# Optimization experiments

Hardware: AMD Instinct MI355X
Metric: run time of the kernel (lower is better)

## Reference

```python
import jax, jax.numpy as jnp
import numpy as np

N_NODES, N_EDGES = 10000, 160000
MUL0, MUL1 = 64, 32  # multiplicities of 0e and 1o in irreps_in
AVG_DEGREE = 16.0

# ---- real-basis Wigner 3j symbols (unit Frobenius norm, as in e3nn) ----
def _su2_gen(l):
    m = np.arange(-l, l + 1)
    Jz = np.diag(m).astype(complex)
    c = np.sqrt(l * (l + 1) - m[:-1] * (m[:-1] + 1))
    Jp = np.zeros((2 * l + 1, 2 * l + 1), complex)
    Jp[np.arange(1, 2 * l + 1), np.arange(2 * l)] = c
    Jm = Jp.conj().T
    return (Jp + Jm) / 2, (Jp - Jm) / 2j, Jz

def _c2r(l):
    U = np.zeros((2 * l + 1, 2 * l + 1), complex)
    s2 = 1 / np.sqrt(2)
    for m in range(-l, l + 1):
        if m > 0:
            U[l + m, l - m] = s2; U[l + m, l + m] = (-1) ** m * s2
        elif m == 0:
            U[l, l] = 1.0
        else:
            U[l + m, l + m] = 1j * s2; U[l + m, l - m] = -1j * (-1) ** m * s2
    return U

def _real_gen(l):
    U = _c2r(l)
    return [np.real(U @ (-1j * J) @ U.conj().T) for J in _su2_gen(l)]

def real_w3j(l1, l2, l3):
    A1, A2, A3 = _real_gen(l1), _real_gen(l2), _real_gen(l3)
    d1, d2, d3 = 2 * l1 + 1, 2 * l2 + 1, 2 * l3 + 1
    I1, I2, I3 = np.eye(d1), np.eye(d2), np.eye(d3)
    M = np.concatenate([
        np.kron(np.kron(A1[k], I2), I3) + np.kron(np.kron(I1, A2[k]), I3)
        + np.kron(np.kron(I1, I2), A3[k]) for k in range(3)], 0)
    v = np.linalg.svd(M)[2][-1]
    v = v / np.linalg.norm(v)
    nz = np.nonzero(np.abs(v) > 1e-8)[0][0]
    if v[nz] < 0:
        v = -v
    return jnp.asarray(v.reshape(d1, d2, d3), dtype=jnp.float32)

W000 = real_w3j(0, 0, 0); W011 = real_w3j(0, 1, 1); W022 = real_w3j(0, 2, 2)
W101 = real_w3j(1, 0, 1); W110 = real_w3j(1, 1, 0); W112 = real_w3j(1, 1, 2)
W121 = real_w3j(1, 2, 1)

# silu second-moment normalization constant (e3nn normalize2mom)
_x, _w = np.polynomial.hermite_e.hermegauss(128)
_s = _x / (1 + np.exp(-_x))
SILU_C = float(1.0 / np.sqrt((_w * _s ** 2).sum() / _w.sum()))
SQ3, SQ5 = float(np.sqrt(3.0)), float(np.sqrt(5.0))


def _forward(node_input, node_attr, edge_attr, edge_length_embedded,
             sc_w0, sc_w1, lin1_w0, lin1_w1, fc_w0, fc_w1,
             lin2_w0, lin2_w1, lin2_w2, edge_src, edge_dst):
    N = node_input.shape[0]
    E = edge_attr.shape[0]
    a = node_attr  # [N,1] scalar (0e) node attribute
    x0 = node_input[:, :MUL0]                       # [N,64]  0e block
    x1 = node_input[:, MUL0:].reshape(N, MUL1, 3)   # [N,32,3] 1o block

    # self connection sc = FullyConnectedTensorProduct(in, attr, out); no 2e path
    s0 = (x0 @ sc_w0) * a / jnp.sqrt(float(MUL0))
    s1 = jnp.einsum('nui,uv->nvi', x1, sc_w1) * a[:, :, None] / jnp.sqrt(float(MUL1))
    s = jnp.concatenate([s0, s1.reshape(N, -1),
                         jnp.zeros((N, 32 * 5), node_input.dtype)], 1)  # [N,320]

    # lin1 = FullyConnectedTensorProduct(in, attr, in)
    y0 = (x0 @ lin1_w0) * a / jnp.sqrt(float(MUL0))
    y1 = jnp.einsum('nui,uv->nvi', x1, lin1_w1) * a[:, :, None] / jnp.sqrt(float(MUL1))

    # radial FC net -> per-edge tensor-product weights [E,320]
    h = jax.nn.silu(edge_length_embedded @ fc_w0 / jnp.sqrt(8.0)) * SILU_C
    w = h @ fc_w1 / jnp.sqrt(64.0)

    xs0 = y0[edge_src][:, :, None]  # [E,64,1]
    xs1 = y1[edge_src]              # [E,32,3]
    e0, e1, e2 = edge_attr[:, :1], edge_attr[:, 1:4], edge_attr[:, 4:9]

    def path(x, e, wgt, C, pw):
        # x:[E,u,d1] e:[E,d2] wgt:[E,u] C:[d1,d2,d3] -> [E,u,d3]
        return pw * jnp.einsum('eui,ej,ijk,eu->euk', x, e, C, wgt)

    # 7 'uvu' instructions; weight slices in instruction order, outputs in sorted
    # irreps_mid order: 64x0e,32x0e,64x1o,32x1o,32x1o,64x2e,32x2e
    k0 = path(xs0, e0, w[:, 0:64],    W000, 1.0)   # 0e x 0e -> 0e, mul 64
    k2 = path(xs0, e1, w[:, 64:128],  W011, SQ3)   # 0e x 1o -> 1o, mul 64
    k5 = path(xs0, e2, w[:, 128:192], W022, SQ5)   # 0e x 2e -> 2e, mul 64
    k3 = path(xs1, e0, w[:, 192:224], W101, SQ3)   # 1o x 0e -> 1o, mul 32
    k1 = path(xs1, e1, w[:, 224:256], W110, 1.0)   # 1o x 1o -> 0e, mul 32
    k6 = path(xs1, e1, w[:, 256:288], W112, SQ5)   # 1o x 1o -> 2e, mul 32
    k4 = path(xs1, e2, w[:, 288:320], W121, SQ3)   # 1o x 2e -> 1o, mul 32
    edge_feat = jnp.concatenate(
        [k0.reshape(E, -1), k1.reshape(E, -1), k2.reshape(E, -1), k3.reshape(E, -1),
         k4.reshape(E, -1), k5.reshape(E, -1), k6.reshape(E, -1)], 1)  # [E,960]

    agg = jax.ops.segment_sum(edge_feat, edge_dst, num_segments=N) / jnp.sqrt(AVG_DEGREE)

    # lin2 = FullyConnectedTensorProduct(mid, attr, out); per-l fused matmuls
    m0 = agg[:, :96]                        # 0e muls 64+32
    m1 = agg[:, 96:480].reshape(N, 128, 3)  # 1o muls 64+32+32
    m2 = agg[:, 480:960].reshape(N, 96, 5)  # 2e muls 64+32
    o0 = (m0 @ lin2_w0) * a / jnp.sqrt(96.0)
    o1 = jnp.einsum('nui,uv->nvi', m1, lin2_w1) * a[:, :, None] / jnp.sqrt(128.0)
    o2 = jnp.einsum('nui,uv->nvi', m2, lin2_w2) * a[:, :, None] / jnp.sqrt(96.0)
    xo = jnp.concatenate([o0, o1.reshape(N, -1), o2.reshape(N, -1)], 1)  # [N,320]

    c_s = jnp.sin(jnp.pi / 8)
    c_x = jnp.cos(jnp.pi / 8)
    mask = jnp.concatenate([jnp.ones(160), jnp.zeros(160)]).astype(node_input.dtype)
    return c_s * s + (1.0 - mask + c_x * mask) * xo


def setup_inputs() -> dict:
    key = jax.random.key(0)
    ks = jax.random.split(key, 16)
    f = jax.random.normal
    return {
        'node_input': f(ks[0], (N_NODES, 160), jnp.float32),
        'node_attr': jnp.ones((N_NODES, 1), jnp.float32),
        'edge_src': jax.random.randint(ks[1], (N_EDGES,), 0, N_NODES, dtype=jnp.int32),
        'edge_dst': jax.random.randint(ks[2], (N_EDGES,), 0, N_NODES, dtype=jnp.int32),
        'edge_attr': f(ks[3], (N_EDGES, 9), jnp.float32),
        'edge_length_embedded': jax.random.uniform(ks[4], (N_EDGES, 8), dtype=jnp.float32),
        'sc_w0': f(ks[5], (64, 64), jnp.float32),
        'sc_w1': f(ks[6], (32, 32), jnp.float32),
        'lin1_w0': f(ks[7], (64, 64), jnp.float32),
        'lin1_w1': f(ks[8], (32, 32), jnp.float32),
        'fc_w0': f(ks[9], (8, 64), jnp.float32),
        'fc_w1': f(ks[10], (64, 320), jnp.float32),
        'lin2_w0': f(ks[11], (96, 64), jnp.float32),
        'lin2_w1': f(ks[12], (128, 32), jnp.float32),
        'lin2_w2': f(ks[13], (96, 32), jnp.float32),
    }


def reference(node_input, node_attr, edge_src, edge_dst, edge_attr, edge_length_embedded,
              sc_w0, sc_w1, lin1_w0, lin1_w1, fc_w0, fc_w1, lin2_w0, lin2_w1, lin2_w2):
    return _forward(node_input, node_attr, edge_attr, edge_length_embedded,
                    sc_w0, sc_w1, lin1_w0, lin1_w1, fc_w0, fc_w1,
                    lin2_w0, lin2_w1, lin2_w2, edge_src, edge_dst)
```

## Files before the change

kernel.cpp:

```cpp
#include <hip/hip_runtime.h>
#include <cstddef>
#include <cstdint>

#define N_NODES 10000
#define N_EDGES 160000

#define RS8    0.35355339059327373f
#define RS32   0.17677669529663687f
#define RS96   0.10206207261596575f
#define RS128  0.08838834764831845f
#define RS3    0.5773502691896258f
#define SQ3_   1.7320508075688772f
#define SQ5_   2.23606797749979f
#define A_     0.18257418583505536f
#define B_     0.31622776601683794f
#define SILU_C_ 1.6765208f
#define CS_    0.3826834323650898f
#define CX_    0.9238795325112867f
#define QDEG   0.25f

typedef __attribute__((ext_vector_type(8))) short bf16x8;
typedef __attribute__((ext_vector_type(4))) float f32x4;

__device__ inline float bf2f(unsigned v) {
  union { unsigned u; float f; } c; c.u = v << 16; return c.f;
}
__device__ inline float bfhi(unsigned v) {
  union { unsigned u; float f; } c; c.u = v & 0xffff0000u; return c.f;
}
__device__ inline unsigned short f2bf(float f) {
  union { float f; unsigned u; } c; c.f = f;
  unsigned r = c.u + 0x7fff + ((c.u >> 16) & 1);
  return (unsigned short)(r >> 16);
}
__device__ inline unsigned pack2bf(float a, float b) {
  return (unsigned)f2bf(a) | ((unsigned)f2bf(b) << 16);
}
__device__ inline float silu_c(float x) {
  return SILU_C_ * x / (1.f + __expf(-x));
}

__global__ void k_init(int* __restrict__ counts, const float* __restrict__ fc1,
                       unsigned short* __restrict__ fc1p,
                       const float* __restrict__ fc0,
                       unsigned short* __restrict__ fc0p) {
  int i = blockIdx.x * blockDim.x + threadIdx.x;
  if (i < N_NODES) counts[i] = 0;
  if (i < 20480) {
    int j = i & 7, q = (i >> 3) & 3, n = (i >> 5) & 15, kq = (i >> 9) & 1, t = i >> 10;
    int k = kq * 32 + q * 8 + j;
    fc1p[i] = f2bf(fc1[k * 320 + t * 16 + n]);
  } else if (i < 20480 + 2048) {
    int ii = i - 20480;
    int j = ii & 7;
    int lane = (ii >> 3) & 63;
    int ch = lane & 15, quad = lane >> 4;
    int nt = ii >> 9;
    int k = quad * 8 + j;
    float v = (k < 8) ? RS8 * fc0[k * 64 + nt * 16 + ch] : 0.f;
    fc0p[ii] = f2bf(v);
  }
}

__global__ void k_hist(const int* __restrict__ edst, int* __restrict__ counts) {
  int e = blockIdx.x * blockDim.x + threadIdx.x;
  if (e < N_EDGES) atomicAdd(&counts[edst[e]], 1);
}

__global__ __launch_bounds__(256) void k_wprep(
    const float* __restrict__ sc_w0, const float* __restrict__ sc_w1,
    const float* __restrict__ w0, const float* __restrict__ w1,
    const float* __restrict__ w2, const float* __restrict__ l1_w0,
    const float* __restrict__ l1_w1, unsigned short* __restrict__ Wp,
    unsigned short* __restrict__ Wyp) {
  int i = blockIdx.x * 256 + threadIdx.x;
  if (i < 358400) {
    int j = i & 7;
    int lane = (i >> 3) & 63;
    int ch = lane & 15, quad = lane >> 4;
    int r = i >> 9;
    int nt = r / 35, ks = r - nt * 35;
    int k = ks * 32 + quad * 8 + j;
    int oc = nt * 16 + ch;
    float v = 0.f;
    if (k < 96) {
      if (oc < 64) v = (CX_ * RS96) * w0[k * 64 + oc];
    } else if (k < 480) {
      int tt = k - 96, u = tt / 3, ii = tt - u * 3;
      if (oc >= 64 && oc < 160) {
        int d = oc - 64, vv = d / 3, jj = d - vv * 3;
        if (jj == ii) v = (CX_ * RS128) * w1[u * 32 + vv];
      }
    } else if (k < 960) {
      int tt = k - 480, u = tt / 5, kk = tt - u * 5;
      if (oc >= 160) {
        int d = oc - 160, vv = d / 5, jj = d - vv * 5;
        if (jj == kk) v = RS96 * w2[u * 32 + vv];
      }
    } else if (k < 1024) {
      int u = k - 960;
      if (oc < 64) v = (CS_ * 0.125f) * sc_w0[u * 64 + oc];
    } else {
      int tt = k - 1024, u = tt / 3, ii = tt - u * 3;
      if (oc >= 64 && oc < 160) {
        int d = oc - 64, vv = d / 3, jj = d - vv * 3;
        if (jj == ii) v = (CS_ * RS32) * sc_w1[u * 32 + vv];
      }
    }
    Wp[i] = f2bf(v);
  } else if (i < 358400 + 30720) {
    int ii2 = i - 358400;
    int j = ii2 & 7;
    int lane = (ii2 >> 3) & 63;
    int ch = lane & 15, quad = lane >> 4;
    int r = ii2 >> 9;
    int nt = r / 5, ks = r - nt * 5;
    int k = ks * 32 + quad * 8 + j;
    int oc = nt * 16 + ch;
    float v = 0.f;
    if (k < 64) {
      if (oc < 64) v = 0.125f * l1_w0[k * 64 + oc];
    } else {
      int tt = k - 64, u = tt / 3, ci = tt - u * 3;
      if (oc >= 64) {
        int d = oc - 64, vv = d >> 2, jj = d & 3;
        if (jj == ci) v = RS32 * l1_w1[u * 32 + vv];
      }
    }
    Wyp[ii2] = f2bf(v);
  }
}

__global__ __launch_bounds__(256) void k_scan(const int* __restrict__ counts,
                                              int* __restrict__ offs,
                                              int* __restrict__ cur,
                                              int* __restrict__ dcur) {
  __shared__ int ps[256];
  __shared__ int dbin[256];
  int t = threadIdx.x;
  dbin[t] = 0;
  int base = t * 40;
  int sum = 0;
  for (int i = 0; i < 40; ++i) {
    int idx = base + i;
    if (idx < N_NODES) sum += counts[idx];
  }
  ps[t] = sum;
  __syncthreads();
  for (int off = 1; off < 256; off <<= 1) {
    int v = (t >= off) ? ps[t - off] : 0;
    __syncthreads();
    ps[t] += v;
    __syncthreads();
  }
  int run = (t == 0) ? 0 : ps[t - 1];
  for (int i = 0; i < 40; ++i) {
    int idx = base + i;
    if (idx < N_NODES) {
      int c = counts[idx];
      offs[idx] = run; cur[idx] = run;
      run += c;
      atomicAdd(&dbin[c < 255 ? c : 255], 1);
    }
  }
  __syncthreads();
  int rb = 255 - t;
  int v = dbin[rb];
  __syncthreads();
  ps[t] = v;
  __syncthreads();
  for (int off = 1; off < 256; off <<= 1) {
    int u = (t >= off) ? ps[t - off] : 0;
    __syncthreads();
    ps[t] += u;
    __syncthreads();
  }
  dcur[rb] = ps[t] - v;
}

__global__ __launch_bounds__(256) void k_perm(
    const int* __restrict__ edst, int* __restrict__ cur,
    const int* __restrict__ counts, const int* __restrict__ offs,
    int* __restrict__ dcur, int* __restrict__ order,
    int* __restrict__ obeg, int* __restrict__ ocnt,
    const float* __restrict__ ele, const float* __restrict__ eattr,
    const int* __restrict__ esrc, float* __restrict__ ed2) {
  __shared__ __align__(16) float sh_ea[256 * 9];
  __shared__ __align__(16) float sh_el[256 * 8];
  int t = threadIdx.x;
  int eb = blockIdx.x * 256;
  int e = eb + t;
  for (int i = t; i < 2304; i += 256) sh_ea[i] = eattr[(size_t)eb * 9 + i];
  {
    const float4* src = (const float4*)(ele + (size_t)eb * 8);
    float4* dst = (float4*)sh_el;
    dst[t] = src[t]; dst[t + 256] = src[t + 256];
  }
  __syncthreads();
  int d = edst[e];
  int p = atomicAdd(&cur[d], 1);
  const float* ea = sh_ea + t * 9;
  const float* el = sh_el + t * 8;
  float4 r0 = {ea[0], ea[1], ea[2], ea[3]};
  float4 r1 = {ea[4], ea[5], ea[6], ea[7]};
  float4 r2 = {ea[8], __int_as_float(esrc[e]), 0.f, 0.f};
  float4 r3 = {el[0], el[1], el[2], el[3]};
  float4 r4 = {el[4], el[5], el[6], el[7]};
  float4* dst = (float4*)(ed2 + (size_t)p * 20);
  dst[0] = r0; dst[1] = r1; dst[2] = r2; dst[3] = r3; dst[4] = r4;
  if (e < N_NODES) {
    int c = counts[e];
    int b = c < 255 ? c : 255;
    int q = atomicAdd(&dcur[b], 1);
    order[q] = e; obeg[q] = offs[e]; ocnt[q] = c;
  }
}

__device__ inline f32x4 wtile(const unsigned short* __restrict__ fc1p,
                              bf16x8 a0, bf16x8 a1, int mrow, int quad, int t) {
  f32x4 acc = {0.f, 0.f, 0.f, 0.f};
  bf16x8 b0 = *(const bf16x8*)(fc1p + ((size_t)((t * 2 + 0) * 16 + mrow) * 4 + quad) * 8);
  bf16x8 b1 = *(const bf16x8*)(fc1p + ((size_t)((t * 2 + 1) * 16 + mrow) * 4 + quad) * 8);
  acc = __builtin_amdgcn_mfma_f32_16x16x32_bf16(b0, a0, acc, 0, 0, 0);
  acc = __builtin_amdgcn_mfma_f32_16x16x32_bf16(b1, a1, acc, 0, 0, 0);
  return acc;
}

struct WgemmShared {
  __align__(16) unsigned short elb[64 * 32];
  __align__(16) unsigned short h[64 * 72];
};

__device__ void w_gemm_body(WgemmShared& sh, int blk,
    const float* __restrict__ ed2, const unsigned short* __restrict__ fc0p,
    const unsigned short* __restrict__ fc1p, unsigned short* __restrict__ wout) {
  int t = threadIdx.x;
  int eb = blk * 64;
  {
    int e = t >> 2, q = t & 3;
    uint4 pk = {0u, 0u, 0u, 0u};
    if (q == 0) {
      const float4* ep = (const float4*)(ed2 + (size_t)(eb + e) * 20 + 12);
      float4 u = ep[0], v = ep[1];
      pk.x = pack2bf(u.x, u.y); pk.y = pack2bf(u.z, u.w);
      pk.z = pack2bf(v.x, v.y); pk.w = pack2bf(v.z, v.w);
    }
    *(uint4*)(sh.elb + e * 32 + q * 8) = pk;
  }
  __syncthreads();

  int wv = t >> 6, lane = t & 63;
  int ch16 = lane & 15, quad = lane >> 4;
  {
    bf16x8 af = *(const bf16x8*)(sh.elb + (wv * 16 + ch16) * 32 + quad * 8);
    bf16x8 b0 = *(const bf16x8*)(fc0p + 0 * 512 + lane * 8);
    bf16x8 b1 = *(const bf16x8*)(fc0p + 1 * 512 + lane * 8);
    bf16x8 b2 = *(const bf16x8*)(fc0p + 2 * 512 + lane * 8);
    bf16x8 b3 = *(const bf16x8*)(fc0p + 3 * 512 + lane * 8);
    f32x4 z = {0.f, 0.f, 0.f, 0.f};
    f32x4 h0 = __builtin_amdgcn_mfma_f32_16x16x32_bf16(b0, af, z, 0, 0, 0);
    f32x4 h1 = __builtin_amdgcn_mfma_f32_16x16x32_bf16(b1, af, z, 0, 0, 0);
    f32x4 h2 = __builtin_amdgcn_mfma_f32_16x16x32_bf16(b2, af, z, 0, 0, 0);
    f32x4 h3 = __builtin_amdgcn_mfma_f32_16x16x32_bf16(b3, af, z, 0, 0, 0);
    unsigned short* hb = sh.h + (wv * 16 + ch16) * 72 + quad * 4;
    uint2 s;
    s.x = pack2bf(silu_c(h0[0]), silu_c(h0[1]));
    s.y = pack2bf(silu_c(h0[2]), silu_c(h0[3]));
    *(uint2*)(hb + 0) = s;
    s.x = pack2bf(silu_c(h1[0]), silu_c(h1[1]));
    s.y = pack2bf(silu_c(h1[2]), silu_c(h1[3]));
    *(uint2*)(hb + 16) = s;
    s.x = pack2bf(silu_c(h2[0]), silu_c(h2[1]));
    s.y = pack2bf(silu_c(h2[2]), silu_c(h2[3]));
    *(uint2*)(hb + 32) = s;
    s.x = pack2bf(silu_c(h3[0]), silu_c(h3[1]));
    s.y = pack2bf(silu_c(h3[2]), silu_c(h3[3]));
    *(uint2*)(hb + 48) = s;
  }
  __syncthreads();

  int m0 = wv * 16;
  int mrow = lane & 15;
  bf16x8 a0 = *(const bf16x8*)(sh.h + (m0 + mrow) * 72 + quad * 8);
  bf16x8 a1 = *(const bf16x8*)(sh.h + (m0 + mrow) * 72 + 32 + quad * 8);
  char* wbase = (char*)wout + (size_t)(eb + m0 + mrow) * 640;
  const float K = 0.125f;
  #pragma unroll
  for (int tt = 0; tt < 4; ++tt) {
    f32x4 Av = wtile(fc1p, a0, a1, mrow, quad, tt);
    f32x4 Bv = wtile(fc1p, a0, a1, mrow, quad, tt + 4);
    uint4 st;
    st.x = pack2bf(Av[0] * K, Bv[0] * K);
    st.y = pack2bf(Av[1] * K, Bv[1] * K);
    st.z = pack2bf(Av[2] * K, Bv[2] * K);
    st.w = pack2bf(Av[3] * K, Bv[3] * K);
    *(uint4*)(wbase + 64 * tt + 16 * quad) = st;
  }
  #pragma unroll
  for (int tt = 8; tt < 12; ++tt) {
    f32x4 Cv = wtile(fc1p, a0, a1, mrow, quad, tt);
    uint2 st;
    st.x = pack2bf(Cv[0] * K, Cv[1] * K);
    st.y = pack2bf(Cv[2] * K, Cv[3] * K);
    *(uint2*)(wbase + 256 + 32 * (tt - 8) + 8 * quad) = st;
  }
  #pragma unroll
  for (int tt = 12; tt < 14; ++tt) {
    f32x4 Dv = wtile(fc1p, a0, a1, mrow, quad, tt);
    f32x4 Ev = wtile(fc1p, a0, a1, mrow, quad, tt + 2);
    f32x4 Fv = wtile(fc1p, a0, a1, mrow, quad, tt + 4);
    f32x4 Gv = wtile(fc1p, a0, a1, mrow, quad, tt + 6);
    char* db = wbase + 384 + 128 * (tt - 12) + 32 * quad;
    uint4 s0, s1;
    s0.x = pack2bf(Dv[0] * K, Ev[0] * K); s0.y = pack2bf(Fv[0] * K, Gv[0] * K);
    s0.z = pack2bf(Dv[1] * K, Ev[1] * K); s0.w = pack2bf(Fv[1] * K, Gv[1] * K);
    s1.x = pack2bf(Dv[2] * K, Ev[2] * K); s1.y = pack2bf(Fv[2] * K, Gv[2] * K);
    s1.z = pack2bf(Dv[3] * K, Ev[3] * K); s1.w = pack2bf(Fv[3] * K, Gv[3] * K);
    *(uint4*)(db) = s0;
    *(uint4*)(db + 16) = s1;
  }
}

__global__ __launch_bounds__(256) void k_mid(
    const float* __restrict__ ed2, const unsigned short* __restrict__ fc0p,
    const unsigned short* __restrict__ fc1p, unsigned short* __restrict__ wout) {
  __shared__ WgemmShared sh;
  w_gemm_body(sh, blockIdx.x, ed2, fc0p, fc1p, wout);
}

#define YSTR 168
__global__ __launch_bounds__(256) void k_npre(
    const float* __restrict__ xin, const float* __restrict__ attr,
    const unsigned short* __restrict__ Wyp, float* __restrict__ y) {
  __shared__ __align__(16) unsigned short Ash[16 * YSTR];
  int t = threadIdx.x;
  int nbase = blockIdx.x * 16;
  for (int idx = t; idx < 16 * 80; idx += 256) {
    int row = idx / 80, c = idx - row * 80;
    const float* xp = xin + (size_t)(nbase + row) * 160 + 2 * c;
    *(unsigned*)(Ash + row * YSTR + 2 * c) = pack2bf(xp[0], xp[1]);
  }
  __syncthreads();
  int wid = t >> 6, lane = t & 63;
  int ch = lane & 15, quad = lane >> 4;
  const unsigned short* arow = Ash + ch * YSTR + quad * 8;
  f32x4 acc0 = {0.f,0.f,0.f,0.f}, acc1 = {0.f,0.f,0.f,0.f}, acc2 = {0.f,0.f,0.f,0.f};
  const unsigned short* wq0 = Wyp + ((size_t)(wid * 3 + 0) * 5 * 64 + lane) * 8;
  const unsigned short* wq1 = Wyp + ((size_t)(wid * 3 + 1) * 5 * 64 + lane) * 8;
  const unsigned short* wq2 = Wyp + ((size_t)(wid * 3 + 2) * 5 * 64 + lane) * 8;
  #pragma unroll
  for (int ks = 0; ks < 5; ++ks) {
    bf16x8 af  = *(const bf16x8*)(arow + ks * 32);
    bf16x8 w0f = *(const bf16x8*)(wq0 + ks * 512);
    bf16x8 w1f = *(const bf16x8*)(wq1 + ks * 512);
    bf16x8 w2f = *(const bf16x8*)(wq2 + ks * 512);
    acc0 = __builtin_amdgcn_mfma_f32_16x16x32_bf16(w0f, af, acc0, 0, 0, 0);
    acc1 = __builtin_amdgcn_mfma_f32_16x16x32_bf16(w1f, af, acc1, 0, 0, 0);
    acc2 = __builtin_amdgcn_mfma_f32_16x16x32_bf16(w2f, af, acc2, 0, 0, 0);
  }
  float a = attr[nbase + ch];
  float* yrow = y + (size_t)(nbase + ch) * 192 + quad * 4;
  { float4 st = {acc0[0]*a, acc0[1]*a, acc0[2]*a, acc0[3]*a};
    *(float4*)(yrow + (wid * 3 + 0) * 16) = st; }
  { float4 st = {acc1[0]*a, acc1[1]*a, acc1[2]*a, acc1[3]*a};
    *(float4*)(yrow + (wid * 3 + 1) * 16) = st; }
  { float4 st = {acc2[0]*a, acc2[1]*a, acc2[2]*a, acc2[3]*a};
    *(float4*)(yrow + (wid * 3 + 2) * 16) = st; }
}

__global__ __launch_bounds__(256) void node_agg(
    const float* __restrict__ y, const float* __restrict__ ed2,
    const unsigned short* __restrict__ wbuf,
    const int* __restrict__ order, const int* __restrict__ obeg,
    const int* __restrict__ ocnt, unsigned short* __restrict__ aggb) {
  int tid = threadIdx.x, wid = tid >> 6, lane = tid & 63, l31 = lane & 31;
  int gw = blockIdx.x * 4 + wid;
  int voY  = 4 * lane;
  int voX  = 256 + 16 * l31;
  int voAB = 4 * lane;
  int voC  = 256 + 2 * lane;
  int voDG = 384 + 8 * l31;

#define E_LOAD(S, idx)                                                         \
  if ((idx) < cnt) {                                                           \
    const float4* ep = (const float4*)(ed2 + (size_t)(beg + (idx)) * 20);      \
    PE0##S = ep[0]; PE1##S = ep[1]; PE2##S = ep[2];                            \
  }
#define V_LOAD(S, idx)                                                         \
  if ((idx) < cnt) {                                                           \
    int srcn = __float_as_int(PE2##S.y);                                       \
    const char* yb = (const char*)y + (size_t)srcn * 768;                      \
    Y##S = *(const float*)(yb + voY);                                          \
    X##S = *(const f32x4*)(yb + voX);                                          \
    const char* wb = (const char*)wbuf + (size_t)(beg + (idx)) * 640;          \
    AB##S = *(const unsigned*)(wb + voAB);                                     \
    Cw##S = *(const unsigned short*)(wb + voC);                                \
    DG##S = *(const uint2*)(wb + voDG);                                        \
  }
#define COMPUTE(S)                                                             \
  {                                                                            \
    float e0 = PE0##S.x, ey = PE0##S.y, ez = PE0##S.z, ex = PE0##S.w;          \
    float q0 = PE1##S.x, q1 = PE1##S.y, q2 = PE1##S.z, q3 = PE1##S.w;          \
    float q4 = PE2##S.x;                                                       \
    float Yv = Y##S, x0 = X##S.x, x1 = X##S.y, x2 = X##S.z;                    \
    float vA = bf2f(AB##S), vB = bfhi(AB##S), vC = bf2f(Cw##S);                \
    float vD = bf2f(DG##S.x), vE = bfhi(DG##S.x);                              \
    float vF = bf2f(DG##S.y), vG = bfhi(DG##S.y);                              \
    aK0 += Yv * e0 * vA;                                                       \
    float tB = Yv * vB; aK2x += tB * ey; aK2y += tB * ez; aK2z += tB * ex;     \
    float tC = Yv * vC;                                                        \
    aK5a += tC * q0; aK5b += tC * q1; aK5c += tC * q2;                         \
    aK5d += tC * q3; aK5e += tC * q4;                                          \
    float t1 = x0 * ey + x1 * ez + x2 * ex; aK1 += (RS3 * vE) * t1;            \
    float s3 = e0 * vD; aK3x += x0 * s3; aK3y += x1 * s3; aK3z += x2 * s3;     \
    float s4 = SQ3_ * vG;                                                      \
    aK4x += s4 * (B_ * (x2 * q0 + x1 * q1 - x0 * q4) - A_ * x0 * q2);          \
    aK4y += s4 * (B_ * (x0 * q1 + x2 * q3) + 2.f * A_ * x1 * q2);              \
    aK4z += s4 * (B_ * (x0 * q0 + x1 * q3 + x2 * q4) - A_ * x2 * q2);          \
    float s6 = SQ5_ * vF;                                                      \
    aK6a += s6 * (-B_ * (x0 * ex + x2 * ey));                                  \
    aK6b += s6 * (-B_ * (x0 * ez + x1 * ey));                                  \
    aK6c += s6 * ( A_ * (x0 * ey + x2 * ex - 2.f * x1 * ez));                  \
    aK6d += s6 * (-B_ * (x1 * ex + x2 * ez));                                  \
    aK6e += s6 * ( B_ * (x0 * ey - x2 * ex));                                  \
  }

  int n = order[gw], beg = obeg[gw], cnt = ocnt[gw];

  float aK0 = 0.f, aK2x = 0.f, aK2y = 0.f, aK2z = 0.f;
  float aK5a = 0.f, aK5b = 0.f, aK5c = 0.f, aK5d = 0.f, aK5e = 0.f;
  float aK1 = 0.f, aK3x = 0.f, aK3y = 0.f, aK3z = 0.f;
  float aK4x = 0.f, aK4y = 0.f, aK4z = 0.f;
  float aK6a = 0.f, aK6b = 0.f, aK6c = 0.f, aK6d = 0.f, aK6e = 0.f;

  float4 PE0a, PE1a, PE2a, PE0b, PE1b, PE2b;
  float Ya, Yb; f32x4 Xa, Xb;
  unsigned ABa, ABb; unsigned short Cwa, Cwb;
  uint2 DGa, DGb;

  E_LOAD(a, 0)
  E_LOAD(b, 1)
  V_LOAD(a, 0)

  int i = 0;
  while (i < cnt) {
    V_LOAD(b, i + 1)
    COMPUTE(a)
    E_LOAD(a, i + 2)
    ++i; if (i >= cnt) break;
    V_LOAD(a, i + 1)
    COMPUTE(b)
    E_LOAD(b, i + 2)
    ++i;
  }

  unsigned short* ag = aggb + (size_t)n * 960;
  ag[lane]           = f2bf(aK0  * QDEG);
  ag[96 + 3 * lane]  = f2bf(aK2x * QDEG);
  ag[97 + 3 * lane]  = f2bf(aK2y * QDEG);
  ag[98 + 3 * lane]  = f2bf(aK2z * QDEG);
  ag[480 + 5 * lane] = f2bf(aK5a * QDEG);
  ag[481 + 5 * lane] = f2bf(aK5b * QDEG);
  ag[482 + 5 * lane] = f2bf(aK5c * QDEG);
  ag[483 + 5 * lane] = f2bf(aK5d * QDEG);
  ag[484 + 5 * lane] = f2bf(aK5e * QDEG);
  if (lane < 32) {
    ag[64 + lane]      = f2bf(aK1  * QDEG);
    ag[288 + 3 * lane] = f2bf(aK3x * QDEG);
    ag[289 + 3 * lane] = f2bf(aK3y * QDEG);
    ag[290 + 3 * lane] = f2bf(aK3z * QDEG);
    ag[384 + 3 * lane] = f2bf(aK4x * QDEG);
    ag[385 + 3 * lane] = f2bf(aK4y * QDEG);
    ag[386 + 3 * lane] = f2bf(aK4z * QDEG);
    ag[800 + 5 * lane] = f2bf(aK6a * QDEG);
    ag[801 + 5 * lane] = f2bf(aK6b * QDEG);
    ag[802 + 5 * lane] = f2bf(aK6c * QDEG);
    ag[803 + 5 * lane] = f2bf(aK6d * QDEG);
    ag[804 + 5 * lane] = f2bf(aK6e * QDEG);
  }
#undef E_LOAD
#undef V_LOAD
#undef COMPUTE
}

#define ASTR 1128
__global__ __launch_bounds__(256) void k_out(
    const unsigned short* __restrict__ aggb, const float* __restrict__ xin,
    const float* __restrict__ attr, const unsigned short* __restrict__ Wp,
    float* __restrict__ out) {
  __shared__ __align__(16) unsigned short Ash[16 * ASTR];
  int t = threadIdx.x;
  int nbase = blockIdx.x * 16;
  for (int idx = t; idx < 16 * 480; idx += 256) {
    int row = idx / 480, c = idx - row * 480;
    *(unsigned*)(Ash + row * ASTR + 2 * c) =
        *(const unsigned*)(aggb + (size_t)(nbase + row) * 960 + 2 * c);
  }
  for (int idx = t; idx < 16 * 80; idx += 256) {
    int row = idx / 80, c = idx - row * 80;
    const float* xp = xin + (size_t)(nbase + row) * 160 + 2 * c;
    *(unsigned*)(Ash + row * ASTR + 960 + 2 * c) = pack2bf(xp[0], xp[1]);
  }
  __syncthreads();

  int wid = t >> 6, lane = t & 63;
  int ch = lane & 15, quad = lane >> 4;
  f32x4 acc0 = {0.f,0.f,0.f,0.f}, acc1 = {0.f,0.f,0.f,0.f};
  f32x4 acc2 = {0.f,0.f,0.f,0.f}, acc3 = {0.f,0.f,0.f,0.f};
  f32x4 acc4 = {0.f,0.f,0.f,0.f};
  const unsigned short* arow = Ash + ch * ASTR + quad * 8;
  const unsigned short* wq0 = Wp + ((size_t)(wid * 5 + 0) * 35 * 64 + lane) * 8;
  const unsigned short* wq1 = Wp + ((size_t)(wid * 5 + 1) * 35 * 64 + lane) * 8;
  const unsigned short* wq2 = Wp + ((size_t)(wid * 5 + 2) * 35 * 64 + lane) * 8;
  const unsigned short* wq3 = Wp + ((size_t)(wid * 5 + 3) * 35 * 64 + lane) * 8;
  const unsigned short* wq4 = Wp + ((size_t)(wid * 5 + 4) * 35 * 64 + lane) * 8;
  for (int ks = 0; ks < 35; ++ks) {
    bf16x8 af = *(const bf16x8*)(arow + ks * 32);
    bf16x8 w0f = *(const bf16x8*)(wq0 + ks * 512);
    bf16x8 w1f = *(const bf16x8*)(wq1 + ks * 512);
    bf16x8 w2f = *(const bf16x8*)(wq2 + ks * 512);
    bf16x8 w3f = *(const bf16x8*)(wq3 + ks * 512);
    bf16x8 w4f = *(const bf16x8*)(wq4 + ks * 512);
    acc0 = __builtin_amdgcn_mfma_f32_16x16x32_bf16(w0f, af, acc0, 0, 0, 0);
    acc1 = __builtin_amdgcn_mfma_f32_16x16x32_bf16(w1f, af, acc1, 0, 0, 0);
    acc2 = __builtin_amdgcn_mfma_f32_16x16x32_bf16(w2f, af, acc2, 0, 0, 0);
    acc3 = __builtin_amdgcn_mfma_f32_16x16x32_bf16(w3f, af, acc3, 0, 0, 0);
    acc4 = __builtin_amdgcn_mfma_f32_16x16x32_bf16(w4f, af, acc4, 0, 0, 0);
  }
  float a = attr[nbase + ch];
  float* orow = out + (size_t)(nbase + ch) * 320 + quad * 4;
  {
    float4 st = {acc0[0]*a, acc0[1]*a, acc0[2]*a, acc0[3]*a};
    *(float4*)(orow + (wid * 5 + 0) * 16) = st;
  }
  {
    float4 st = {acc1[0]*a, acc1[1]*a, acc1[2]*a, acc1[3]*a};
    *(float4*)(orow + (wid * 5 + 1) * 16) = st;
  }
  {
    float4 st = {acc2[0]*a, acc2[1]*a, acc2[2]*a, acc2[3]*a};
    *(float4*)(orow + (wid * 5 + 2) * 16) = st;
  }
  {
    float4 st = {acc3[0]*a, acc3[1]*a, acc3[2]*a, acc3[3]*a};
    *(float4*)(orow + (wid * 5 + 3) * 16) = st;
  }
  {
    float4 st = {acc4[0]*a, acc4[1]*a, acc4[2]*a, acc4[3]*a};
    *(float4*)(orow + (wid * 5 + 4) * 16) = st;
  }
}

extern "C" void kernel_launch(void* const* d_in, const int* in_sizes, int n_in,
                              void* d_out, int out_size, void* d_ws, size_t ws_size,
                              hipStream_t stream) {
  const float* node_input = (const float*)d_in[0];
  const float* node_attr  = (const float*)d_in[1];
  const int*   edge_src   = (const int*)d_in[2];
  const int*   edge_dst   = (const int*)d_in[3];
  const float* edge_attr  = (const float*)d_in[4];
  const float* ele        = (const float*)d_in[5];
  const float* sc_w0      = (const float*)d_in[6];
  const float* sc_w1      = (const float*)d_in[7];
  const float* l1_w0      = (const float*)d_in[8];
  const float* l1_w1      = (const float*)d_in[9];
  const float* fc_w0      = (const float*)d_in[10];
  const float* fc_w1      = (const float*)d_in[11];
  const float* l2_w0      = (const float*)d_in[12];
  const float* l2_w1      = (const float*)d_in[13];
  const float* l2_w2      = (const float*)d_in[14];
  float* out = (float*)d_out;

  char* base = (char*)d_ws;
  float* y              = (float*)(base);
  unsigned short* wbuf  = (unsigned short*)(base + 7680000);
  float* ed2            = (float*)(base + 110080000);
  int* counts           = (int*)(base + 122880000);
  int* offs             = (int*)(base + 122920000);
  int* cur              = (int*)(base + 122960000);
  int* order            = (int*)(base + 123000000);
  int* obeg             = (int*)(base + 123040000);
  int* ocnt             = (int*)(base + 123080000);
  int* dcur             = (int*)(base + 123120000);
  unsigned short* fc1p  = (unsigned short*)(base + 123121024);
  unsigned short* aggb  = (unsigned short*)(base + 123162624);
  unsigned short* Wp    = (unsigned short*)(base + 142362624);
  unsigned short* Wyp   = (unsigned short*)(base + 143079424);
  unsigned short* fc0p  = (unsigned short*)(base + 143140864);

  hipLaunchKernelGGL(k_init, dim3(88), dim3(256), 0, stream, counts, fc_w1, fc1p,
                     fc_w0, fc0p);
  hipLaunchKernelGGL(k_wprep, dim3(1520), dim3(256), 0, stream,
                     sc_w0, sc_w1, l2_w0, l2_w1, l2_w2, l1_w0, l1_w1, Wp, Wyp);
  hipLaunchKernelGGL(k_hist, dim3((N_EDGES + 255) / 256), dim3(256), 0, stream,
                     edge_dst, counts);
  hipLaunchKernelGGL(k_scan, dim3(1), dim3(256), 0, stream, counts, offs, cur, dcur);
  hipLaunchKernelGGL(k_perm, dim3(N_EDGES / 256), dim3(256), 0, stream,
                     edge_dst, cur, counts, offs, dcur, order, obeg, ocnt,
                     ele, edge_attr, edge_src, ed2);
  hipLaunchKernelGGL(k_npre, dim3(625), dim3(256), 0, stream,
                     node_input, node_attr, Wyp, y);
  hipLaunchKernelGGL(k_mid, dim3(2500), dim3(256), 0, stream,
                     ed2, fc0p, fc1p, wbuf);
  hipLaunchKernelGGL(node_agg, dim3(2500), dim3(256), 0, stream,
                     y, ed2, wbuf, order, obeg, ocnt, aggb);
  hipLaunchKernelGGL(k_out, dim3(625), dim3(256), 0, stream,
                     aggb, node_input, node_attr, Wp, out);
}
```

Measured before the change: 205.0 us.

## Merge prep kernels, fuse npre into mid GEMM, split edge record array

Merges the init, histogram and weight-prep kernels into a single launch, with the counts zeroing moved to a memset. Folds the node pre-linear into the edge-weight GEMM kernel through block-index dispatch and a shared-memory union. Splits the 20-float sorted edge record into a 12-float part used by aggregation and an 8-float part used by the GEMM. This cuts launch count and inter-kernel bubbles and trims the bytes each consumer reads, at the cost of a larger shared-memory footprint in the fused kernel and mixed work types within one grid.

New measurement: 198.2 us (median of 2 runs). 1.03x faster.

```diff
diff --git a/kernel.cpp b/kernel.cpp
--- a/kernel.cpp
+++ b/kernel.cpp
@@ -40,40 +40,40 @@
   return SILU_C_ * x / (1.f + __expf(-x));
 }
 
-__global__ void k_init(int* __restrict__ counts, const float* __restrict__ fc1,
-                       unsigned short* __restrict__ fc1p,
-                       const float* __restrict__ fc0,
-                       unsigned short* __restrict__ fc0p) {
-  int i = blockIdx.x * blockDim.x + threadIdx.x;
-  if (i < N_NODES) counts[i] = 0;
-  if (i < 20480) {
-    int j = i & 7, q = (i >> 3) & 3, n = (i >> 5) & 15, kq = (i >> 9) & 1, t = i >> 10;
-    int k = kq * 32 + q * 8 + j;
-    fc1p[i] = f2bf(fc1[k * 320 + t * 16 + n]);
-  } else if (i < 20480 + 2048) {
-    int ii = i - 20480;
-    int j = ii & 7;
-    int lane = (ii >> 3) & 63;
-    int ch = lane & 15, quad = lane >> 4;
-    int nt = ii >> 9;
-    int k = quad * 8 + j;
-    float v = (k < 8) ? RS8 * fc0[k * 64 + nt * 16 + ch] : 0.f;
-    fc0p[ii] = f2bf(v);
-  }
-}
-
-__global__ void k_hist(const int* __restrict__ edst, int* __restrict__ counts) {
-  int e = blockIdx.x * blockDim.x + threadIdx.x;
-  if (e < N_EDGES) atomicAdd(&counts[edst[e]], 1);
-}
-
-__global__ __launch_bounds__(256) void k_wprep(
+__global__ __launch_bounds__(256) void k_prep(
+    const int* __restrict__ edst, int* __restrict__ counts,
+    const float* __restrict__ fc1, unsigned short* __restrict__ fc1p,
+    const float* __restrict__ fc0, unsigned short* __restrict__ fc0p,
     const float* __restrict__ sc_w0, const float* __restrict__ sc_w1,
     const float* __restrict__ w0, const float* __restrict__ w1,
     const float* __restrict__ w2, const float* __restrict__ l1_w0,
     const float* __restrict__ l1_w1, unsigned short* __restrict__ Wp,
     unsigned short* __restrict__ Wyp) {
-  int i = blockIdx.x * 256 + threadIdx.x;
+  int b = blockIdx.x, t = threadIdx.x;
+  if (b < 625) {
+    int e = b * 256 + t;
+    if (e < N_EDGES) atomicAdd(&counts[edst[e]], 1);
+    return;
+  }
+  if (b < 713) {
+    int i = (b - 625) * 256 + t;
+    if (i < 20480) {
+      int j = i & 7, q = (i >> 3) & 3, n = (i >> 5) & 15, kq = (i >> 9) & 1, tt = i >> 10;
+      int k = kq * 32 + q * 8 + j;
+      fc1p[i] = f2bf(fc1[k * 320 + tt * 16 + n]);
+    } else if (i < 22528) {
+      int ii = i - 20480;
+      int j = ii & 7;
+      int lane = (ii >> 3) & 63;
+      int ch = lane & 15, quad = lane >> 4;
+      int nt = ii >> 9;
+      int k = quad * 8 + j;
+      float v = (k < 8) ? RS8 * fc0[k * 64 + nt * 16 + ch] : 0.f;
+      fc0p[ii] = f2bf(v);
+    }
+    return;
+  }
+  int i = (b - 713) * 256 + t;
   if (i < 358400) {
     int j = i & 7;
     int lane = (i >> 3) & 63;
@@ -184,7 +184,8 @@
     int* __restrict__ dcur, int* __restrict__ order,
     int* __restrict__ obeg, int* __restrict__ ocnt,
     const float* __restrict__ ele, const float* __restrict__ eattr,
-    const int* __restrict__ esrc, float* __restrict__ ed2) {
+    const int* __restrict__ esrc, float* __restrict__ ed2a,
+    float* __restrict__ ed2b) {
   __shared__ __align__(16) float sh_ea[256 * 9];
   __shared__ __align__(16) float sh_el[256 * 8];
   int t = threadIdx.x;
@@ -204,10 +205,12 @@
   float4 r0 = {ea[0], ea[1], ea[2], ea[3]};
   float4 r1 = {ea[4], ea[5], ea[6], ea[7]};
   float4 r2 = {ea[8], __int_as_float(esrc[e]), 0.f, 0.f};
+  float4* da = (float4*)(ed2a + (size_t)p * 12);
+  da[0] = r0; da[1] = r1; da[2] = r2;
   float4 r3 = {el[0], el[1], el[2], el[3]};
   float4 r4 = {el[4], el[5], el[6], el[7]};
-  float4* dst = (float4*)(ed2 + (size_t)p * 20);
-  dst[0] = r0; dst[1] = r1; dst[2] = r2; dst[3] = r3; dst[4] = r4;
+  float4* db = (float4*)(ed2b + (size_t)p * 8);
+  db[0] = r3; db[1] = r4;
   if (e < N_NODES) {
     int c = counts[e];
     int b = c < 255 ? c : 255;
@@ -232,7 +235,7 @@
 };
 
 __device__ void w_gemm_body(WgemmShared& sh, int blk,
-    const float* __restrict__ ed2, const unsigned short* __restrict__ fc0p,
+    const float* __restrict__ ed2b, const unsigned short* __restrict__ fc0p,
     const unsigned short* __restrict__ fc1p, unsigned short* __restrict__ wout) {
   int t = threadIdx.x;
   int eb = blk * 64;
@@ -240,7 +243,7 @@
     int e = t >> 2, q = t & 3;
     uint4 pk = {0u, 0u, 0u, 0u};
     if (q == 0) {
-      const float4* ep = (const float4*)(ed2 + (size_t)(eb + e) * 20 + 12);
+      const float4* ep = (const float4*)(ed2b + (size_t)(eb + e) * 8);
       float4 u = ep[0], v = ep[1];
       pk.x = pack2bf(u.x, u.y); pk.y = pack2bf(u.z, u.w);
       pk.z = pack2bf(v.x, v.y); pk.w = pack2bf(v.z, v.w);
@@ -321,20 +324,12 @@
   }
 }
 
-__global__ __launch_bounds__(256) void k_mid(
-    const float* __restrict__ ed2, const unsigned short* __restrict__ fc0p,
-    const unsigned short* __restrict__ fc1p, unsigned short* __restrict__ wout) {
-  __shared__ WgemmShared sh;
-  w_gemm_body(sh, blockIdx.x, ed2, fc0p, fc1p, wout);
-}
-
 #define YSTR 168
-__global__ __launch_bounds__(256) void k_npre(
+__device__ void npre_body(unsigned short* Ash, int blk,
     const float* __restrict__ xin, const float* __restrict__ attr,
     const unsigned short* __restrict__ Wyp, float* __restrict__ y) {
-  __shared__ __align__(16) unsigned short Ash[16 * YSTR];
   int t = threadIdx.x;
-  int nbase = blockIdx.x * 16;
+  int nbase = blk * 16;
   for (int idx = t; idx < 16 * 80; idx += 256) {
     int row = idx / 80, c = idx - row * 80;
     const float* xp = xin + (size_t)(nbase + row) * 160 + 2 * c;
@@ -368,8 +363,24 @@
     *(float4*)(yrow + (wid * 3 + 2) * 16) = st; }
 }
 
+__global__ __launch_bounds__(256) void k_midpre(
+    const float* __restrict__ ed2b, const unsigned short* __restrict__ fc0p,
+    const unsigned short* __restrict__ fc1p, unsigned short* __restrict__ wout,
+    const float* __restrict__ xin, const float* __restrict__ attr,
+    const unsigned short* __restrict__ Wyp, float* __restrict__ y) {
+  __shared__ union ShU {
+    WgemmShared w;
+    unsigned short ash[16 * YSTR];
+  } sh;
+  if (blockIdx.x < 2500) {
+    w_gemm_body(sh.w, blockIdx.x, ed2b, fc0p, fc1p, wout);
+  } else {
+    npre_body(sh.ash, blockIdx.x - 2500, xin, attr, Wyp, y);
+  }
+}
+
 __global__ __launch_bounds__(256) void node_agg(
-    const float* __restrict__ y, const float* __restrict__ ed2,
+    const float* __restrict__ y, const float* __restrict__ ed2a,
     const unsigned short* __restrict__ wbuf,
     const int* __restrict__ order, const int* __restrict__ obeg,
     const int* __restrict__ ocnt, unsigned short* __restrict__ aggb) {
@@ -383,7 +394,7 @@
 
 #define E_LOAD(S, idx)                                                         \
   if ((idx) < cnt) {                                                           \
-    const float4* ep = (const float4*)(ed2 + (size_t)(beg + (idx)) * 20);      \
+    const float4* ep = (const float4*)(ed2a + (size_t)(beg + (idx)) * 12);     \
     PE0##S = ep[0]; PE1##S = ep[1]; PE2##S = ep[2];                            \
   }
 #define V_LOAD(S, idx)                                                         \
@@ -574,7 +585,8 @@
   char* base = (char*)d_ws;
   float* y              = (float*)(base);
   unsigned short* wbuf  = (unsigned short*)(base + 7680000);
-  float* ed2            = (float*)(base + 110080000);
+  float* ed2a           = (float*)(base + 110080000);
+  float* ed2b           = (float*)(base + 117760000);
   int* counts           = (int*)(base + 122880000);
   int* offs             = (int*)(base + 122920000);
   int* cur              = (int*)(base + 122960000);
@@ -588,22 +600,18 @@
   unsigned short* Wyp   = (unsigned short*)(base + 143079424);
   unsigned short* fc0p  = (unsigned short*)(base + 143140864);
 
-  hipLaunchKernelGGL(k_init, dim3(88), dim3(256), 0, stream, counts, fc_w1, fc1p,
-                     fc_w0, fc0p);
-  hipLaunchKernelGGL(k_wprep, dim3(1520), dim3(256), 0, stream,
+  hipMemsetAsync(counts, 0, N_NODES * sizeof(int), stream);
+  hipLaunchKernelGGL(k_prep, dim3(2233), dim3(256), 0, stream,
+                     edge_dst, counts, fc_w1, fc1p, fc_w0, fc0p,
                      sc_w0, sc_w1, l2_w0, l2_w1, l2_w2, l1_w0, l1_w1, Wp, Wyp);
-  hipLaunchKernelGGL(k_hist, dim3((N_EDGES + 255) / 256), dim3(256), 0, stream,
-                     edge_dst, counts);
   hipLaunchKernelGGL(k_scan, dim3(1), dim3(256), 0, stream, counts, offs, cur, dcur);
   hipLaunchKernelGGL(k_perm, dim3(N_EDGES / 256), dim3(256), 0, stream,
                      edge_dst, cur, counts, offs, dcur, order, obeg, ocnt,
-                     ele, edge_attr, edge_src, ed2);
-  hipLaunchKernelGGL(k_npre, dim3(625), dim3(256), 0, stream,
-                     node_input, node_attr, Wyp, y);
-  hipLaunchKernelGGL(k_mid, dim3(2500), dim3(256), 0, stream,
-                     ed2, fc0p, fc1p, wbuf);
+                     ele, edge_attr, edge_src, ed2a, ed2b);
+  hipLaunchKernelGGL(k_midpre, dim3(3125), dim3(256), 0, stream,
+                     ed2b, fc0p, fc1p, wbuf, node_input, node_attr, Wyp, y);
   hipLaunchKernelGGL(node_agg, dim3(2500), dim3(256), 0, stream,
-                     y, ed2, wbuf, order, obeg, ocnt, aggb);
+                     y, ed2a, wbuf, order, obeg, ocnt, aggb);
   hipLaunchKernelGGL(k_out, dim3(625), dim3(256), 0, stream,
                      aggb, node_input, node_attr, Wp, out);
 }
```
